# Optimization experiments

Measured on AMD Instinct MI355X. Metric: run time of the kernel, lower is better.

## Reference

```python
import jax, jax.numpy as jnp
import numpy as np

HID = 256  # LSTM hidden size hard-coded in the module


def _lstm_dir(x, wih, whh, b):
    # x: (N, T, I) -> (N, T, HID); PyTorch gate order i, f, g, o
    xw = jnp.einsum('nti,gi->ntg', x, wih) + b  # precompute input projection
    h0 = jnp.zeros((x.shape[0], whh.shape[1]), x.dtype)

    def step(carry, xt):
        h, c = carry
        g = xt + h @ whh.T
        i, f, gg, o = jnp.split(g, 4, axis=-1)
        c = jax.nn.sigmoid(f) * c + jax.nn.sigmoid(i) * jnp.tanh(gg)
        h = jax.nn.sigmoid(o) * jnp.tanh(c)
        return (h, c), h

    _, ys = jax.lax.scan(step, (h0, h0), jnp.swapaxes(xw, 0, 1))
    return jnp.swapaxes(ys, 0, 1)


def _bilstm(x, wf, uf, bf, wb, ub, bb):
    fwd = _lstm_dir(x, wf, uf, bf)
    bwd = _lstm_dir(x[:, ::-1], wb, ub, bb)[:, ::-1]
    return jnp.concatenate([fwd, bwd], axis=-1)  # (N, T, 2*HID)


def _renet2d(x, vp, hp, cw, cb):
    # Faithful to Renet2d.forward: vertical LSTM scans along W for each row of H,
    # horizontal LSTM scans along H for each column of W, then 1x1 conv.
    N, C, H, W = x.shape
    # original: transpose(1,3) then x[:,:,i,:] over H -> seq axis W, features C
    v_in = jnp.transpose(x, (0, 2, 3, 1)).reshape(N * H, W, C)
    v_out = _bilstm(v_in, *vp).reshape(N, H, W, 2 * HID)
    # torch.stack(temp, dim=2) -> (N, W, H, 512)
    s = jnp.transpose(v_out, (0, 2, 1, 3))
    h_in = s.reshape(N * W, H, 2 * HID)
    h_out = _bilstm(h_in, *hp).reshape(N, W, H, 2 * HID)
    # stack(dim=3) then transpose(1,2) -> (N, 512, H, W)
    y = jnp.transpose(h_out, (0, 3, 2, 1))
    return jnp.einsum('nchw,oc->nohw', y, cw) + cb[None, :, None, None]


def reference(x, v_wih_f, v_whh_f, v_b_f, v_wih_b, v_whh_b, v_b_b,
              h_wih_f, h_whh_f, h_b_f, h_wih_b, h_whh_b, h_b_b,
              c2_w, c2_b, c3_w, c3_b):
    vp = (v_wih_f, v_whh_f, v_b_f, v_wih_b, v_whh_b, v_b_b)
    hp = (h_wih_f, h_whh_f, h_b_f, h_wih_b, h_whh_b, h_b_b)
    B, C, D, H, W = x.shape
    r2d = lambda z: _renet2d(z, vp, hp, c2_w, c2_b)
    # NOTE: the source reuses Renet2d_D for all three stages (Renet2d_W/H are dead).
    # stage 1: python loop over D slicing dim 2 -> fold D into batch
    t = r2d(jnp.transpose(x, (0, 2, 1, 3, 4)).reshape(B * D, C, H, W)).reshape(B, D, C, H, W)
    x = jnp.transpose(t, (0, 2, 1, 3, 4))
    # stage 2: source loops range(w) but slices dim 3 (H); valid because H == W
    t = r2d(jnp.transpose(x, (0, 3, 1, 2, 4)).reshape(B * H, C, D, W)).reshape(B, H, C, D, W)
    x = jnp.transpose(t, (0, 2, 3, 1, 4))
    # stage 3: loops range(h) slicing dim 4 (W)
    t = r2d(jnp.transpose(x, (0, 4, 1, 2, 3)).reshape(B * W, C, D, H)).reshape(B, W, C, D, H)
    x = jnp.transpose(t, (0, 2, 3, 4, 1))
    # Conv3d 1x1x1
    return jnp.einsum('bcdhw,oc->bodhw', x, c3_w) + c3_b[None, :, None, None, None]


def setup_inputs() -> dict:
    key = jax.random.key(0)
    ks = jax.random.split(key, 17)
    B, C, S, O = 2, 64, 16, 64
    G = 4 * HID
    sc = 0.08

    def n(k, shape):
        return jax.random.normal(k, shape, jnp.float32) * sc

    return {
        'x': jax.random.normal(ks[0], (B, C, S, S, S), jnp.float32),
        # vertical LSTM (input C) fwd/bwd directions; b = b_ih + b_hh fused
        'v_wih_f': n(ks[1], (G, C)), 'v_whh_f': n(ks[2], (G, HID)), 'v_b_f': n(ks[3], (G,)),
        'v_wih_b': n(ks[4], (G, C)), 'v_whh_b': n(ks[5], (G, HID)), 'v_b_b': n(ks[6], (G,)),
        # horizontal LSTM (input 512)
        'h_wih_f': n(ks[7], (G, 2 * HID)), 'h_whh_f': n(ks[8], (G, HID)), 'h_b_f': n(ks[9], (G,)),
        'h_wih_b': n(ks[10], (G, 2 * HID)), 'h_whh_b': n(ks[11], (G, HID)), 'h_b_b': n(ks[12], (G,)),
        # Conv2d(512, in_channel, 1) inside Renet2d_D and Conv3d(in, out, 1)
        'c2_w': n(ks[13], (C, 2 * HID)), 'c2_b': n(ks[14], (C,)),
        'c3_w': n(ks[15], (O, C)), 'c3_b': n(ks[16], (O,)),
    }
```

## Files before the change

### kernel.cpp

```cpp
#include <hip/hip_runtime.h>
#include <hip/hip_bf16.h>
#include <hip/hip_fp16.h>


typedef __attribute__((ext_vector_type(8))) short bf16x8;
typedef __attribute__((ext_vector_type(4))) float f32x4;
typedef __attribute__((ext_vector_type(4))) unsigned int u32x4;
typedef __attribute__((ext_vector_type(2))) unsigned int u32x2;

#define AGENT __HIP_MEMORY_SCOPE_AGENT

__device__ __forceinline__ unsigned short f2bf(float f) {
    unsigned int u = __float_as_uint(f);
    u += 0x7fffu + ((u >> 16) & 1u);
    return (unsigned short)(u >> 16);
}

struct CastW { const float* src[9]; unsigned short* dst[9]; int n[9]; int L[9]; int perm[9]; };
__global__ void k_castw(CastW j) {
    const int a = blockIdx.y;
    const int i = blockIdx.x * 256 + threadIdx.x;
    if (i >= j.n[a]) return;
    const int L = j.L[a];
    const int r = i >> L, c = i & ((1 << L) - 1);
    const int dr = j.perm[a] ? ((r & 255) * 4 + (r >> 8)) : r;
    j.dst[a][(dr << L) | c] = f2bf(j.src[a][i]);
}
struct CastB { const float* src[4]; float* dst[4]; };
__global__ void k_castb(CastB j) {
    const int a = blockIdx.y;
    const int i = blockIdx.x * 256 + threadIdx.x;
    j.dst[a][(i & 255) * 4 + (i >> 8)] = j.src[a][i];
}

__global__ void k_gather(const float* __restrict__ X, unsigned short* __restrict__ vin,
                         int sm, int sa, int sb) {
    const int seq = blockIdx.x;
    const int n = seq >> 4, a = seq & 15;
    const size_t base = (size_t)(n >> 4) * 64 * 4096 + (size_t)sm * (n & 15) + (size_t)sa * a;
    for (int idx = threadIdx.x; idx < 1024; idx += 256) {
        const int c = idx & 63, b = idx >> 6;
        vin[((size_t)seq * 16 + b) * 64 + c] = f2bf(X[base + (size_t)c * 4096 + (size_t)sb * b]);
    }
}

__global__ __launch_bounds__(256) void k_gemm(const unsigned short* __restrict__ A, int K,
        const unsigned short* __restrict__ W0, const unsigned short* __restrict__ W1,
        const float* __restrict__ bias0, const float* __restrict__ bias1,
        __half* __restrict__ C, int ldc, int nvalid,
        int mode, float* __restrict__ out5d, int sm, int sa, int sb) {
    __shared__ unsigned short Alds[128 * 56];
    __shared__ unsigned short Blds[128 * 56];
    const unsigned short* W = blockIdx.z ? W1 : W0;
    const float* bias = blockIdx.z ? bias1 : bias0;
    C += (size_t)blockIdx.z * 8192 * ldc;
    const int m0 = blockIdx.x * 128, n0 = blockIdx.y * 128;
    const int tid = threadIdx.x;
    const int lane = tid & 63, wid = tid >> 6;
    const int wr = wid >> 1, wc = wid & 1;
    const int fl = lane & 15, kk = (lane >> 4) * 8;
    f32x4 acc[4][4];
    #pragma unroll
    for (int mi = 0; mi < 4; mi++)
        #pragma unroll
        for (int ni = 0; ni < 4; ni++) { f32x4 z = {0.f,0.f,0.f,0.f}; acc[mi][ni] = z; }

    for (int k0 = 0; k0 < K; k0 += 32) {
        __syncthreads();
        #pragma unroll
        for (int h = 0; h < 2; h++) {
            const int cid = tid + h * 256;
            const int row = cid >> 2, c4 = cid & 3;
            *(u32x4*)&Alds[row * 56 + c4 * 8] = *(const u32x4*)(A + (size_t)(m0 + row) * K + k0 + c4 * 8);
            *(u32x4*)&Blds[row * 56 + c4 * 8] = *(const u32x4*)(W + (size_t)(n0 + row) * K + k0 + c4 * 8);
        }
        __syncthreads();
        bf16x8 af[4], bfb[4];
        #pragma unroll
        for (int i = 0; i < 4; i++) {
            af[i]  = *(const bf16x8*)&Alds[(wr * 64 + i * 16 + fl) * 56 + kk];
            bfb[i] = *(const bf16x8*)&Blds[(wc * 64 + i * 16 + fl) * 56 + kk];
        }
        #pragma unroll
        for (int mi = 0; mi < 4; mi++)
            #pragma unroll
            for (int ni = 0; ni < 4; ni++)
                acc[mi][ni] = __builtin_amdgcn_mfma_f32_16x16x32_bf16(af[mi], bfb[ni], acc[mi][ni], 0, 0, 0);
    }
    const int rl = (lane >> 4) * 4;
    #pragma unroll
    for (int ni = 0; ni < 4; ni++) {
        const int col = n0 + wc * 64 + ni * 16 + fl;
        if (col < nvalid) {
            const float bs = bias[col];
            #pragma unroll
            for (int mi = 0; mi < 4; mi++) {
                const int row = m0 + wr * 64 + mi * 16 + rl;
                #pragma unroll
                for (int j = 0; j < 4; j++) {
                    const float v = acc[mi][ni][j] + bs;
                    if (mode) {
                        const int r = row + j;
                        const int n_ = r >> 8, b_ = (r >> 4) & 15, a_ = r & 15;
                        out5d[(size_t)(n_ >> 4) * 262144 + (size_t)sm * (n_ & 15) +
                              (size_t)sa * a_ + (size_t)sb * b_ + (size_t)col * 4096] = v;
                    } else {
                        C[(size_t)(row + j) * ldc + col] = __float2half(v);
                    }
                }
            }
        }
    }
}

__global__ __launch_bounds__(512, 2) void k_scan(const __half* __restrict__ xw,
        const unsigned short* __restrict__ whh_f, const unsigned short* __restrict__ whh_b,
        unsigned short* __restrict__ out, int out_mode,
        unsigned long long* __restrict__ HX, unsigned int* __restrict__ FLG, int phase) {
    __shared__ __align__(16) char gbuf[512 * 40];
    __shared__ __align__(16) char hbuf[16 * 512];
    const int tid = threadIdx.x;
    const int lane = tid & 63, w = tid >> 6;
    const int fl = lane & 15, fh = lane >> 4;
    const int st = blockIdx.x, dir = blockIdx.y, kh = blockIdx.z;
    const int seq0 = st * 16;
    const unsigned short* whh_k = (dir ? whh_b : whh_f) + (size_t)kh * 512 * 256;
    const __half* xwd = xw + (size_t)dir * (8192 * 1024);
    const int C0g = kh * 512 + w * 64;
    const int slot = ((dir * 32 + st) * 2 + kh);
    unsigned long long* hx_me = HX + (size_t)slot * 1024;
    const unsigned long long* hx_p = HX + (size_t)(slot ^ 1) * 1024;
    unsigned int* flg_me = FLG + slot * 64;
    unsigned int* flg_p  = FLG + (slot ^ 1) * 64;
    const unsigned int base = 16u * (unsigned int)phase;
    const int kOwnB = kh * 4;
    const int kParB = (1 - kh) * 4;

    #pragma unroll
    for (int i = 0; i < 4; i++) ((unsigned int*)hbuf)[tid + i * 512] = 0u;

    bf16x8 wown[4][4], wpar[4][4];
    #pragma unroll
    for (int nt = 0; nt < 4; nt++) {
        const unsigned short* rowp = whh_k + (size_t)(w * 64 + nt * 16 + fl) * 256 + fh * 8;
        #pragma unroll
        for (int i = 0; i < 4; i++) {
            wown[nt][i] = *(const bf16x8*)(rowp + (kOwnB + i) * 32);
            wpar[nt][i] = *(const bf16x8*)(rowp + (kParB + i) * 32);
        }
    }

    const int li = lane & 15, ls = lane >> 4;
    const int khalf = w * 16 + li;
    const int kglob = kh * 128 + khalf;
    float c_reg[4] = {0.f, 0.f, 0.f, 0.f};

    int tt = dir ? 15 : 0;
    const int tstep = dir ? -1 : 1;

    unsigned int xh[4][2], xhn[4][2];
    #pragma unroll
    for (int nt = 0; nt < 4; nt++)
        #pragma unroll
        for (int j2 = 0; j2 < 2; j2++) {
            const size_t b_ = ((size_t)(seq0 + fh * 4 + j2 * 2) * 16 + tt) * 1024 + C0g + nt * 16 + fl;
            const unsigned short h0 = __half_as_ushort(xwd[b_]);
            const unsigned short h1 = __half_as_ushort(xwd[b_ + 16 * 1024]);
            xh[nt][j2] = (unsigned int)h0 | ((unsigned int)h1 << 16);
        }

    __syncthreads();

    for (int t = 0; t < 16; t++) {
        if (t > 0) {
            const int ttp = tt - tstep;
            const int s = tid >> 5, q = tid & 31;
            const int ba = (s * 512 + (kh * 128 + q * 4) * 2) ^ ((s & 7) << 4);
            const u32x2 hv = *(const u32x2*)(hbuf + ba);
            const size_t row = out_mode ? ((size_t)(seq0 + s) * 16 + ttp)
                                        : ((size_t)st * 256 + (size_t)ttp * 16 + s);
            *(u32x2*)(out + row * 512 + dir * 256 + kh * 128 + q * 4) = hv;
        }
        bf16x8 afr[4];
        #pragma unroll
        for (int i = 0; i < 4; i++) {
            const int ba = (fl * 512 + (kOwnB + i) * 64 + fh * 16) ^ ((fl & 7) << 4);
            afr[i] = *(const bf16x8*)(hbuf + ba);
        }
        f32x4 acc[4];
        #pragma unroll
        for (int nt = 0; nt < 4; nt++) {
            acc[nt][0] = __half2float(__ushort_as_half((unsigned short)(xh[nt][0] & 0xffff)));
            acc[nt][1] = __half2float(__ushort_as_half((unsigned short)(xh[nt][0] >> 16)));
            acc[nt][2] = __half2float(__ushort_as_half((unsigned short)(xh[nt][1] & 0xffff)));
            acc[nt][3] = __half2float(__ushort_as_half((unsigned short)(xh[nt][1] >> 16)));
            #pragma unroll
            for (int i = 0; i < 4; i++)
                acc[nt] = __builtin_amdgcn_mfma_f32_16x16x32_bf16(afr[i], wown[nt][i], acc[nt], 0, 0, 0);
        }
        if (t > 0) {
            if (tid == 0) {
                const unsigned int want = base + (unsigned int)t;
                while (atomicAdd(flg_p, 0u) < want) __builtin_amdgcn_s_sleep(1);
            }
            asm volatile("s_barrier" ::: "memory");
            const unsigned long long pv =
                __hip_atomic_load(hx_p + (((t - 1) & 1) * 512 + tid), __ATOMIC_RELAXED, AGENT);
            const int kl = tid >> 2, sl0 = (tid & 3) * 4;
            const int kp = (1 - kh) * 128 + kl;
            #pragma unroll
            for (int e = 0; e < 4; e++) {
                const int s = sl0 + e;
                *(unsigned short*)(hbuf + ((s * 512 + kp * 2) ^ ((s & 7) << 4))) =
                    (unsigned short)(pv >> (16 * e));
            }
        }
        asm volatile("s_waitcnt lgkmcnt(0)\n\ts_barrier" ::: "memory");

        const int tn = (t < 15) ? tt + tstep : tt;
        #pragma unroll
        for (int nt = 0; nt < 4; nt++)
            #pragma unroll
            for (int j2 = 0; j2 < 2; j2++) {
                const size_t b_ = ((size_t)(seq0 + fh * 4 + j2 * 2) * 16 + tn) * 1024 + C0g + nt * 16 + fl;
                const unsigned short h0 = __half_as_ushort(xwd[b_]);
                const unsigned short h1 = __half_as_ushort(xwd[b_ + 16 * 1024]);
                xhn[nt][j2] = (unsigned int)h0 | ((unsigned int)h1 << 16);
            }

        #pragma unroll
        for (int i = 0; i < 4; i++) {
            const int ba = (fl * 512 + (kParB + i) * 64 + fh * 16) ^ ((fl & 7) << 4);
            afr[i] = *(const bf16x8*)(hbuf + ba);
        }
        #pragma unroll
        for (int nt = 0; nt < 4; nt++) {
            #pragma unroll
            for (int i = 0; i < 4; i++)
                acc[nt] = __builtin_amdgcn_mfma_f32_16x16x32_bf16(afr[i], wpar[nt][i], acc[nt], 0, 0, 0);
            const int coll = w * 64 + nt * 16 + fl;
            const unsigned int lo = (unsigned int)__half_as_ushort(__float2half(acc[nt][0])) |
                                    ((unsigned int)__half_as_ushort(__float2half(acc[nt][1])) << 16);
            const unsigned int hi = (unsigned int)__half_as_ushort(__float2half(acc[nt][2])) |
                                    ((unsigned int)__half_as_ushort(__float2half(acc[nt][3])) << 16);
            u32x2 pk = {lo, hi};
            *(u32x2*)(gbuf + coll * 40 + fh * 8) = pk;
        }

        float gv[4][4];
        const int colbase = w * 64 + 4 * li;
        #pragma unroll
        for (int g = 0; g < 4; g++) {
            const u32x2 a = *(const u32x2*)(gbuf + (colbase + g) * 40 + ls * 8);
            gv[g][0] = __half2float(__ushort_as_half((unsigned short)(a[0] & 0xffff)));
            gv[g][1] = __half2float(__ushort_as_half((unsigned short)(a[0] >> 16)));
            gv[g][2] = __half2float(__ushort_as_half((unsigned short)(a[1] & 0xffff)));
            gv[g][3] = __half2float(__ushort_as_half((unsigned short)(a[1] >> 16)));
        }
        unsigned long long hpack = 0ull;
        #pragma unroll
        for (int p2 = 0; p2 < 4; p2++) {
            const float ig = 1.f / (1.f + __expf(-gv[0][p2]));
            const float fg = 1.f / (1.f + __expf(-gv[1][p2]));
            const float e2 = __expf(2.f * gv[2][p2]);
            const float gg = 1.f - 2.f / (e2 + 1.f);
            const float og = 1.f / (1.f + __expf(-gv[3][p2]));
            const float c = fg * c_reg[p2] + ig * gg;
            c_reg[p2] = c;
            const float e2c = __expf(2.f * c);
            const float hv = og * (1.f - 2.f / (e2c + 1.f));
            const unsigned short hb = f2bf(hv);
            const int s = ls * 4 + p2;
            *(unsigned short*)(hbuf + ((s * 512 + kglob * 2) ^ ((s & 7) << 4))) = hb;
            hpack |= ((unsigned long long)hb) << (16 * p2);
        }

        if (t < 15)
            __hip_atomic_store(hx_me + ((t & 1) * 512 + khalf * 4 + ls), hpack, __ATOMIC_RELAXED, AGENT);
        #pragma unroll
        for (int nt = 0; nt < 4; nt++) { xh[nt][0] = xhn[nt][0]; xh[nt][1] = xhn[nt][1]; }
        tt = tn;
        __syncthreads();
        if (t < 15 && tid == 0)
            atomicExch(flg_me, base + (unsigned int)(t + 1));
    }
    {
        const int s = tid >> 5, q = tid & 31;
        const int ba = (s * 512 + (kh * 128 + q * 4) * 2) ^ ((s & 7) << 4);
        const u32x2 hv = *(const u32x2*)(hbuf + ba);
        const size_t row = out_mode ? ((size_t)(seq0 + s) * 16 + tt)
                                    : ((size_t)st * 256 + (size_t)tt * 16 + s);
        *(u32x2*)(out + row * 512 + dir * 256 + kh * 128 + q * 4) = hv;
    }
}

__global__ __launch_bounds__(256) void k_conv3f(const __half* __restrict__ CONV,
        const float* __restrict__ w, const float* __restrict__ bias, float* __restrict__ out) {
    __shared__ float xl[64 * 32];
    __shared__ float wl[64 * 64];
    const int bb = blockIdx.y;
    const int p0 = blockIdx.x * 32;
    const int tid = threadIdx.x;
    for (int i = tid; i < 64 * 32; i += 256) {
        const int c = i & 63, pp = i >> 6;
        const int p = p0 + pp;
        const int n_ = bb * 16 + (p & 15), b_ = (p >> 4) & 15, a_ = (p >> 8) & 15;
        const int r = (n_ * 16 + b_) * 16 + a_;
        xl[c * 32 + pp] = __half2float(CONV[(size_t)r * 64 + c]);
    }
    for (int i = tid; i < 64 * 64; i += 256) wl[i] = w[i];
    __syncthreads();
    const int pp = tid & 31, og = tid >> 5;
    #pragma unroll
    for (int oj = 0; oj < 8; oj++) {
        const int o = og * 8 + oj;
        float acc = bias[o];
        #pragma unroll 16
        for (int c = 0; c < 64; c++) acc += xl[c * 32 + pp] * wl[o * 64 + c];
        out[((size_t)bb * 64 + o) * 4096 + p0 + pp] = acc;
    }
}

extern "C" void kernel_launch(void* const* d_in, const int* in_sizes, int n_in,
                              void* d_out, int out_size, void* d_ws, size_t ws_size,
                              hipStream_t stream) {
    (void)in_sizes; (void)n_in; (void)out_size; (void)ws_size;
    const float* x     = (const float*)d_in[0];
    const float* vwihf = (const float*)d_in[1];
    const float* vwhhf = (const float*)d_in[2];
    const float* vbf   = (const float*)d_in[3];
    const float* vwihb = (const float*)d_in[4];
    const float* vwhhb = (const float*)d_in[5];
    const float* vbb   = (const float*)d_in[6];
    const float* hwihf = (const float*)d_in[7];
    const float* hwhhf = (const float*)d_in[8];
    const float* hbf   = (const float*)d_in[9];
    const float* hwihb = (const float*)d_in[10];
    const float* hwhhb = (const float*)d_in[11];
    const float* hbb   = (const float*)d_in[12];
    const float* c2w   = (const float*)d_in[13];
    const float* c2b   = (const float*)d_in[14];
    const float* c3w   = (const float*)d_in[15];
    const float* c3b   = (const float*)d_in[16];

    char* p = (char*)d_ws;
    auto alloc = [&](size_t bytes) { char* r = p; p += (bytes + 255) & ~((size_t)255); return r; };
    unsigned short* bVWIHf = (unsigned short*)alloc((size_t)1024 * 64 * 2);
    unsigned short* bVWIHb = (unsigned short*)alloc((size_t)1024 * 64 * 2);
    unsigned short* bVWHHf = (unsigned short*)alloc((size_t)1024 * 256 * 2);
    unsigned short* bVWHHb = (unsigned short*)alloc((size_t)1024 * 256 * 2);
    unsigned short* bHWIHf = (unsigned short*)alloc((size_t)1024 * 512 * 2);
    unsigned short* bHWIHb = (unsigned short*)alloc((size_t)1024 * 512 * 2);
    unsigned short* bHWHHf = (unsigned short*)alloc((size_t)1024 * 256 * 2);
    unsigned short* bHWHHb = (unsigned short*)alloc((size_t)1024 * 256 * 2);
    unsigned short* bC2W   = (unsigned short*)alloc((size_t)128 * 512 * 2);
    float* pVBf = (float*)alloc(1024 * 4);
    float* pVBb = (float*)alloc(1024 * 4);
    float* pHBf = (float*)alloc(1024 * 4);
    float* pHBb = (float*)alloc(1024 * 4);
    unsigned long long* HX = (unsigned long long*)alloc((size_t)128 * 8192);
    unsigned int* FLG = (unsigned int*)alloc((size_t)128 * 256);
    float* XA = (float*)alloc((size_t)524288 * 4);
    float* XB = (float*)alloc((size_t)524288 * 4);
    unsigned short* VIN = (unsigned short*)alloc((size_t)8192 * 64 * 2);
    __half* XW = (__half*)alloc((size_t)2 * 8192 * 1024 * 2);
    unsigned short* S_   = (unsigned short*)alloc((size_t)8192 * 512 * 2);
    unsigned short* HOUT = (unsigned short*)alloc((size_t)8192 * 512 * 2);
    __half* CONV = (__half*)VIN;

    hipMemsetAsync(bC2W, 0, (size_t)128 * 512 * 2, stream);
    hipMemsetAsync(FLG, 0, (size_t)128 * 256, stream);
    CastW cw;
    const float* srcs[9] = {vwihf, vwihb, vwhhf, vwhhb, hwihf, hwihb, hwhhf, hwhhb, c2w};
    unsigned short* dsts[9] = {bVWIHf, bVWIHb, bVWHHf, bVWHHb, bHWIHf, bHWIHb, bHWHHf, bHWHHb, bC2W};
    const int ns[9] = {65536, 65536, 262144, 262144, 524288, 524288, 262144, 262144, 32768};
    const int Ls[9] = {6, 6, 8, 8, 9, 9, 8, 8, 9};
    const int pm[9] = {1, 1, 1, 1, 1, 1, 1, 1, 0};
    for (int i = 0; i < 9; i++) { cw.src[i] = srcs[i]; cw.dst[i] = dsts[i]; cw.n[i] = ns[i]; cw.L[i] = Ls[i]; cw.perm[i] = pm[i]; }
    k_castw<<<dim3(2048, 9), 256, 0, stream>>>(cw);
    CastB cb;
    cb.src[0] = vbf; cb.dst[0] = pVBf;
    cb.src[1] = vbb; cb.dst[1] = pVBb;
    cb.src[2] = hbf; cb.dst[2] = pHBf;
    cb.src[3] = hbb; cb.dst[3] = pHBb;
    k_castb<<<dim3(4, 4), 256, 0, stream>>>(cb);

    const int SMs[3] = {256, 16, 1}, SAs[3] = {16, 256, 256}, SBs[3] = {1, 1, 16};
    for (int s = 0; s < 3; s++) {
        const float* Xin = (s == 0) ? x : ((s == 1) ? XA : XB);
        float* Xout = (s == 0) ? XA : XB;
        k_gather<<<512, 256, 0, stream>>>(Xin, VIN, SMs[s], SAs[s], SBs[s]);
        k_gemm<<<dim3(64, 8, 2), 256, 0, stream>>>(VIN, 64, bVWIHf, bVWIHb, pVBf, pVBb,
                                                   XW, 1024, 1024, 0, nullptr, 0, 0, 0);
        k_scan<<<dim3(32, 2, 2), 512, 0, stream>>>(XW, bVWHHf, bVWHHb, S_, 0, HX, FLG, s * 2 + 0);
        k_gemm<<<dim3(64, 8, 2), 256, 0, stream>>>(S_, 512, bHWIHf, bHWIHb, pHBf, pHBb,
                                                   XW, 1024, 1024, 0, nullptr, 0, 0, 0);
        k_scan<<<dim3(32, 2, 2), 512, 0, stream>>>(XW, bHWHHf, bHWHHb, HOUT, 1, HX, FLG, s * 2 + 1);
        if (s < 2)
            k_gemm<<<dim3(64, 1, 1), 256, 0, stream>>>(HOUT, 512, bC2W, bC2W, c2b, c2b,
                                                       CONV, 64, 64, 1, Xout, SMs[s], SAs[s], SBs[s]);
        else
            k_gemm<<<dim3(64, 1, 1), 256, 0, stream>>>(HOUT, 512, bC2W, bC2W, c2b, c2b,
                                                       CONV, 64, 64, 0, nullptr, 0, 0, 0);
    }
    k_conv3f<<<dim3(128, 2), 256, 0, stream>>>(CONV, c3w, c3b, (float*)d_out);
}
```

Before: 591.0 us.

## Add producer warp for cross-block h exchange in LSTM scan; async LDS loads in GEMM

The scan kernel gains a ninth wavefront that waits on the partner block's flag, reads its half of the hidden state and writes it into a double-buffered LDS h buffer, signalling compute waves through a per-step shared flag instead of a block-wide barrier. The intent is to overlap the inter-block handoff latency with the own-half MFMA work and the input prefetch. Separately, the GEMM tile loads switch to global_load_lds with an XOR swizzle instead of padded register-staged copies. Risks include the spin-wait on LDS flags, the barrier count matching between producer and compute waves, and occupancy dropping to one 576-thread block per CU.

```diff
diff --git a/kernel.cpp b/kernel.cpp
--- a/kernel.cpp
+++ b/kernel.cpp
@@ -14,6 +14,10 @@
     unsigned int u = __float_as_uint(f);
     u += 0x7fffu + ((u >> 16) & 1u);
     return (unsigned short)(u >> 16);
+}
+__device__ __forceinline__ void gload16(const void* g, void* l) {
+    __builtin_amdgcn_global_load_lds((const __attribute__((address_space(1))) unsigned int*)g,
+                                     (__attribute__((address_space(3))) unsigned int*)l, 16, 0, 0);
 }
 
 struct CastW { const float* src[9]; unsigned short* dst[9]; int n[9]; int L[9]; int perm[9]; };
@@ -49,8 +53,8 @@
         const float* __restrict__ bias0, const float* __restrict__ bias1,
         __half* __restrict__ C, int ldc, int nvalid,
         int mode, float* __restrict__ out5d, int sm, int sa, int sb) {
-    __shared__ unsigned short Alds[128 * 56];
-    __shared__ unsigned short Blds[128 * 56];
+    __shared__ unsigned short Alds[128 * 32];
+    __shared__ unsigned short Blds[128 * 32];
     const unsigned short* W = blockIdx.z ? W1 : W0;
     const float* bias = blockIdx.z ? bias1 : bias0;
     C += (size_t)blockIdx.z * 8192 * ldc;
@@ -58,28 +62,29 @@
     const int tid = threadIdx.x;
     const int lane = tid & 63, wid = tid >> 6;
     const int wr = wid >> 1, wc = wid & 1;
-    const int fl = lane & 15, kk = (lane >> 4) * 8;
+    const int fl = lane & 15, fh = lane >> 4;
     f32x4 acc[4][4];
     #pragma unroll
     for (int mi = 0; mi < 4; mi++)
         #pragma unroll
         for (int ni = 0; ni < 4; ni++) { f32x4 z = {0.f,0.f,0.f,0.f}; acc[mi][ni] = z; }
 
+    const int srow = wid * 32 + (lane >> 2);
+    const int swz = ((lane & 3) ^ ((lane >> 2) & 3)) * 8;
+
     for (int k0 = 0; k0 < K; k0 += 32) {
         __syncthreads();
-        #pragma unroll
-        for (int h = 0; h < 2; h++) {
-            const int cid = tid + h * 256;
-            const int row = cid >> 2, c4 = cid & 3;
-            *(u32x4*)&Alds[row * 56 + c4 * 8] = *(const u32x4*)(A + (size_t)(m0 + row) * K + k0 + c4 * 8);
-            *(u32x4*)&Blds[row * 56 + c4 * 8] = *(const u32x4*)(W + (size_t)(n0 + row) * K + k0 + c4 * 8);
-        }
+        gload16(A + (size_t)(m0 + srow) * K + k0 + swz,      &Alds[(wid * 32) * 32]);
+        gload16(A + (size_t)(m0 + srow + 16) * K + k0 + swz, &Alds[(wid * 32 + 16) * 32]);
+        gload16(W + (size_t)(n0 + srow) * K + k0 + swz,      &Blds[(wid * 32) * 32]);
+        gload16(W + (size_t)(n0 + srow + 16) * K + k0 + swz, &Blds[(wid * 32 + 16) * 32]);
         __syncthreads();
         bf16x8 af[4], bfb[4];
+        const int rc = (fh ^ (fl & 3)) * 8;
         #pragma unroll
         for (int i = 0; i < 4; i++) {
-            af[i]  = *(const bf16x8*)&Alds[(wr * 64 + i * 16 + fl) * 56 + kk];
-            bfb[i] = *(const bf16x8*)&Blds[(wc * 64 + i * 16 + fl) * 56 + kk];
+            af[i]  = *(const bf16x8*)&Alds[(wr * 64 + i * 16 + fl) * 32 + rc];
+            bfb[i] = *(const bf16x8*)&Blds[(wc * 64 + i * 16 + fl) * 32 + rc];
         }
         #pragma unroll
         for (int mi = 0; mi < 4; mi++)
@@ -87,7 +92,7 @@
             for (int ni = 0; ni < 4; ni++)
                 acc[mi][ni] = __builtin_amdgcn_mfma_f32_16x16x32_bf16(af[mi], bfb[ni], acc[mi][ni], 0, 0, 0);
     }
-    const int rl = (lane >> 4) * 4;
+    const int rl = fh * 4;
     #pragma unroll
     for (int ni = 0; ni < 4; ni++) {
         const int col = n0 + wc * 64 + ni * 16 + fl;
@@ -113,12 +118,13 @@
     }
 }
 
-__global__ __launch_bounds__(512, 2) void k_scan(const __half* __restrict__ xw,
+__global__ __launch_bounds__(576, 1) void k_scan(const __half* __restrict__ xw,
         const unsigned short* __restrict__ whh_f, const unsigned short* __restrict__ whh_b,
         unsigned short* __restrict__ out, int out_mode,
         unsigned long long* __restrict__ HX, unsigned int* __restrict__ FLG, int phase) {
     __shared__ __align__(16) char gbuf[512 * 40];
-    __shared__ __align__(16) char hbuf[16 * 512];
+    __shared__ __align__(16) char hbuf[2 * 8192];
+    __shared__ int sflag[16];
     const int tid = threadIdx.x;
     const int lane = tid & 63, w = tid >> 6;
     const int fl = lane & 15, fh = lane >> 4;
@@ -126,7 +132,6 @@
     const int seq0 = st * 16;
     const unsigned short* whh_k = (dir ? whh_b : whh_f) + (size_t)kh * 512 * 256;
     const __half* xwd = xw + (size_t)dir * (8192 * 1024);
-    const int C0g = kh * 512 + w * 64;
     const int slot = ((dir * 32 + st) * 2 + kh);
     unsigned long long* hx_me = HX + (size_t)slot * 1024;
     const unsigned long long* hx_p = HX + (size_t)(slot ^ 1) * 1024;
@@ -136,18 +141,67 @@
     const int kOwnB = kh * 4;
     const int kParB = (1 - kh) * 4;
 
-    #pragma unroll
-    for (int i = 0; i < 4; i++) ((unsigned int*)hbuf)[tid + i * 512] = 0u;
+    if (tid < 16) sflag[tid] = 0;
+    for (int i = tid; i < 2048; i += 576) ((unsigned int*)(hbuf + 8192))[i] = 0u;
 
     bf16x8 wown[4][4], wpar[4][4];
-    #pragma unroll
-    for (int nt = 0; nt < 4; nt++) {
-        const unsigned short* rowp = whh_k + (size_t)(w * 64 + nt * 16 + fl) * 256 + fh * 8;
-        #pragma unroll
-        for (int i = 0; i < 4; i++) {
-            wown[nt][i] = *(const bf16x8*)(rowp + (kOwnB + i) * 32);
-            wpar[nt][i] = *(const bf16x8*)(rowp + (kParB + i) * 32);
-        }
+    unsigned int xh[4][2], xhn[4][2];
+    const int C0g = kh * 512 + w * 64;
+    int tt = dir ? 15 : 0;
+    const int tstep = dir ? -1 : 1;
+    if (w < 8) {
+        #pragma unroll
+        for (int nt = 0; nt < 4; nt++) {
+            const unsigned short* rowp = whh_k + (size_t)(w * 64 + nt * 16 + fl) * 256 + fh * 8;
+            #pragma unroll
+            for (int i = 0; i < 4; i++) {
+                wown[nt][i] = *(const bf16x8*)(rowp + (kOwnB + i) * 32);
+                wpar[nt][i] = *(const bf16x8*)(rowp + (kParB + i) * 32);
+            }
+        }
+        #pragma unroll
+        for (int nt = 0; nt < 4; nt++)
+            #pragma unroll
+            for (int j2 = 0; j2 < 2; j2++) {
+                const size_t b_ = ((size_t)(seq0 + fh * 4 + j2 * 2) * 16 + tt) * 1024 + C0g + nt * 16 + fl;
+                const unsigned short h0 = __half_as_ushort(xwd[b_]);
+                const unsigned short h1 = __half_as_ushort(xwd[b_ + 16 * 1024]);
+                xh[nt][j2] = (unsigned int)h0 | ((unsigned int)h1 << 16);
+            }
+    }
+    __syncthreads();
+
+    if (w == 8) {
+        for (int t = 0; t < 16; t++) {
+            if (t > 0) {
+                if (lane == 0) {
+                    const unsigned int want = base + (unsigned int)t;
+                    while (atomicAdd(flg_p, 0u) < want) __builtin_amdgcn_s_sleep(1);
+                }
+                const unsigned long long* src = hx_p + ((t - 1) & 1) * 512;
+                unsigned long long pv[8];
+                #pragma unroll
+                for (int e = 0; e < 8; e++)
+                    pv[e] = __hip_atomic_load(src + lane + e * 64, __ATOMIC_RELAXED, AGENT);
+                char* hwbuf = hbuf + ((t - 1) & 1) * 8192;
+                #pragma unroll
+                for (int e = 0; e < 8; e++) {
+                    const int idx = lane + e * 64;
+                    const int kl = idx >> 2, sl0 = (idx & 3) * 4;
+                    const int kp = (1 - kh) * 128 + kl;
+                    #pragma unroll
+                    for (int e2 = 0; e2 < 4; e2++) {
+                        const int s = sl0 + e2;
+                        *(unsigned short*)(hwbuf + ((s * 512 + kp * 2) ^ ((s & 7) << 4))) =
+                            (unsigned short)(pv[e] >> (16 * e2));
+                    }
+                }
+                asm volatile("s_waitcnt lgkmcnt(0)" ::: "memory");
+                if (lane == 0) *(volatile int*)&sflag[t] = 1;
+            }
+            __syncthreads();
+        }
+        return;
     }
 
     const int li = lane & 15, ls = lane >> 4;
@@ -155,28 +209,14 @@
     const int kglob = kh * 128 + khalf;
     float c_reg[4] = {0.f, 0.f, 0.f, 0.f};
 
-    int tt = dir ? 15 : 0;
-    const int tstep = dir ? -1 : 1;
-
-    unsigned int xh[4][2], xhn[4][2];
-    #pragma unroll
-    for (int nt = 0; nt < 4; nt++)
-        #pragma unroll
-        for (int j2 = 0; j2 < 2; j2++) {
-            const size_t b_ = ((size_t)(seq0 + fh * 4 + j2 * 2) * 16 + tt) * 1024 + C0g + nt * 16 + fl;
-            const unsigned short h0 = __half_as_ushort(xwd[b_]);
-            const unsigned short h1 = __half_as_ushort(xwd[b_ + 16 * 1024]);
-            xh[nt][j2] = (unsigned int)h0 | ((unsigned int)h1 << 16);
-        }
-
-    __syncthreads();
-
     for (int t = 0; t < 16; t++) {
+        const char* hread = hbuf + ((t - 1) & 1) * 8192;
+        char* hwr = hbuf + (t & 1) * 8192;
         if (t > 0) {
             const int ttp = tt - tstep;
             const int s = tid >> 5, q = tid & 31;
             const int ba = (s * 512 + (kh * 128 + q * 4) * 2) ^ ((s & 7) << 4);
-            const u32x2 hv = *(const u32x2*)(hbuf + ba);
+            const u32x2 hv = *(const u32x2*)(hread + ba);
             const size_t row = out_mode ? ((size_t)(seq0 + s) * 16 + ttp)
                                         : ((size_t)st * 256 + (size_t)ttp * 16 + s);
             *(u32x2*)(out + row * 512 + dir * 256 + kh * 128 + q * 4) = hv;
@@ -185,7 +225,7 @@
         #pragma unroll
         for (int i = 0; i < 4; i++) {
             const int ba = (fl * 512 + (kOwnB + i) * 64 + fh * 16) ^ ((fl & 7) << 4);
-            afr[i] = *(const bf16x8*)(hbuf + ba);
+            afr[i] = *(const bf16x8*)(hread + ba);
         }
         f32x4 acc[4];
         #pragma unroll
@@ -198,25 +238,6 @@
             for (int i = 0; i < 4; i++)
                 acc[nt] = __builtin_amdgcn_mfma_f32_16x16x32_bf16(afr[i], wown[nt][i], acc[nt], 0, 0, 0);
         }
-        if (t > 0) {
-            if (tid == 0) {
-                const unsigned int want = base + (unsigned int)t;
-                while (atomicAdd(flg_p, 0u) < want) __builtin_amdgcn_s_sleep(1);
-            }
-            asm volatile("s_barrier" ::: "memory");
-            const unsigned long long pv =
-                __hip_atomic_load(hx_p + (((t - 1) & 1) * 512 + tid), __ATOMIC_RELAXED, AGENT);
-            const int kl = tid >> 2, sl0 = (tid & 3) * 4;
-            const int kp = (1 - kh) * 128 + kl;
-            #pragma unroll
-            for (int e = 0; e < 4; e++) {
-                const int s = sl0 + e;
-                *(unsigned short*)(hbuf + ((s * 512 + kp * 2) ^ ((s & 7) << 4))) =
-                    (unsigned short)(pv >> (16 * e));
-            }
-        }
-        asm volatile("s_waitcnt lgkmcnt(0)\n\ts_barrier" ::: "memory");
-
         const int tn = (t < 15) ? tt + tstep : tt;
         #pragma unroll
         for (int nt = 0; nt < 4; nt++)
@@ -227,11 +248,15 @@
                 const unsigned short h1 = __half_as_ushort(xwd[b_ + 16 * 1024]);
                 xhn[nt][j2] = (unsigned int)h0 | ((unsigned int)h1 << 16);
             }
-
+        if (t > 0) {
+            volatile int* sf = (volatile int*)&sflag[t];
+            while (*sf == 0) { }
+            asm volatile("" ::: "memory");
+        }
         #pragma unroll
         for (int i = 0; i < 4; i++) {
             const int ba = (fl * 512 + (kParB + i) * 64 + fh * 16) ^ ((fl & 7) << 4);
-            afr[i] = *(const bf16x8*)(hbuf + ba);
+            afr[i] = *(const bf16x8*)(hread + ba);
         }
         #pragma unroll
         for (int nt = 0; nt < 4; nt++) {
@@ -246,7 +271,6 @@
             u32x2 pk = {lo, hi};
             *(u32x2*)(gbuf + coll * 40 + fh * 8) = pk;
         }
-
         float gv[4][4];
         const int colbase = w * 64 + 4 * li;
         #pragma unroll
@@ -271,10 +295,9 @@
             const float hv = og * (1.f - 2.f / (e2c + 1.f));
             const unsigned short hb = f2bf(hv);
             const int s = ls * 4 + p2;
-            *(unsigned short*)(hbuf + ((s * 512 + kglob * 2) ^ ((s & 7) << 4))) = hb;
+            *(unsigned short*)(hwr + ((s * 512 + kglob * 2) ^ ((s & 7) << 4))) = hb;
             hpack |= ((unsigned long long)hb) << (16 * p2);
         }
-
         if (t < 15)
             __hip_atomic_store(hx_me + ((t & 1) * 512 + khalf * 4 + ls), hpack, __ATOMIC_RELAXED, AGENT);
         #pragma unroll
@@ -287,7 +310,7 @@
     {
         const int s = tid >> 5, q = tid & 31;
         const int ba = (s * 512 + (kh * 128 + q * 4) * 2) ^ ((s & 7) << 4);
-        const u32x2 hv = *(const u32x2*)(hbuf + ba);
+        const u32x2 hv = *(const u32x2*)(hbuf + 8192 + ba);
         const size_t row = out_mode ? ((size_t)(seq0 + s) * 16 + tt)
                                     : ((size_t)st * 256 + (size_t)tt * 16 + s);
         *(u32x2*)(out + row * 512 + dir * 256 + kh * 128 + q * 4) = hv;
@@ -392,10 +415,10 @@
         k_gather<<<512, 256, 0, stream>>>(Xin, VIN, SMs[s], SAs[s], SBs[s]);
         k_gemm<<<dim3(64, 8, 2), 256, 0, stream>>>(VIN, 64, bVWIHf, bVWIHb, pVBf, pVBb,
                                                    XW, 1024, 1024, 0, nullptr, 0, 0, 0);
-        k_scan<<<dim3(32, 2, 2), 512, 0, stream>>>(XW, bVWHHf, bVWHHb, S_, 0, HX, FLG, s * 2 + 0);
+        k_scan<<<dim3(32, 2, 2), 576, 0, stream>>>(XW, bVWHHf, bVWHHb, S_, 0, HX, FLG, s * 2 + 0);
         k_gemm<<<dim3(64, 8, 2), 256, 0, stream>>>(S_, 512, bHWIHf, bHWIHb, pHBf, pHBb,
                                                    XW, 1024, 1024, 0, nullptr, 0, 0, 0);
-        k_scan<<<dim3(32, 2, 2), 512, 0, stream>>>(XW, bHWHHf, bHWHHb, HOUT, 1, HX, FLG, s * 2 + 1);
+        k_scan<<<dim3(32, 2, 2), 576, 0, stream>>>(XW, bHWHHf, bHWHHb, HOUT, 1, HX, FLG, s * 2 + 1);
         if (s < 2)
             k_gemm<<<dim3(64, 1, 1), 256, 0, stream>>>(HOUT, 512, bC2W, bC2W, c2b, c2b,
                                                        CONV, 64, 64, 1, Xout, SMs[s], SAs[s], SBs[s]);
```

After: 799.1 us. 1.35x slower.

## Use direct global-to-LDS loads with XOR swizzle in GEMM; tile gather via LDS

Applied to the files above, without the earlier changes.

The GEMM tile loads now use global_load_lds (16-byte direct-to-LDS) into an unpadded LDS layout. An XOR swizzle is applied on both the load and the fragment read to avoid bank conflicts, which removes the register round-trip and shrinks the LDS footprint. The gather kernel now stages the transposed bf16 data through shared memory so that global writes are coalesced 8-byte stores instead of scattered 2-byte stores. The direct-load path depends on per-wave contiguous LDS placement matching the swizzle, so any indexing mistake would silently corrupt results.

```diff
diff --git a/kernel.cpp b/kernel.cpp
--- a/kernel.cpp
+++ b/kernel.cpp
@@ -14,6 +14,10 @@
     unsigned int u = __float_as_uint(f);
     u += 0x7fffu + ((u >> 16) & 1u);
     return (unsigned short)(u >> 16);
+}
+__device__ __forceinline__ void gload16(const void* g, void* l) {
+    __builtin_amdgcn_global_load_lds((const __attribute__((address_space(1))) unsigned int*)g,
+                                     (__attribute__((address_space(3))) unsigned int*)l, 16, 0, 0);
 }
 
 struct CastW { const float* src[9]; unsigned short* dst[9]; int n[9]; int L[9]; int perm[9]; };
@@ -35,13 +39,24 @@
 
 __global__ void k_gather(const float* __restrict__ X, unsigned short* __restrict__ vin,
                          int sm, int sa, int sb) {
+    __shared__ unsigned short sd[16 * 68];
     const int seq = blockIdx.x;
     const int n = seq >> 4, a = seq & 15;
     const size_t base = (size_t)(n >> 4) * 64 * 4096 + (size_t)sm * (n & 15) + (size_t)sa * a;
-    for (int idx = threadIdx.x; idx < 1024; idx += 256) {
-        const int c = idx & 63, b = idx >> 6;
-        vin[((size_t)seq * 16 + b) * 64 + c] = f2bf(X[base + (size_t)c * 4096 + (size_t)sb * b]);
-    }
+    const int t = threadIdx.x;
+    #pragma unroll
+    for (int j = 0; j < 4; j++) {
+        const int i = t + j * 256;
+        const int c = i >> 4, b = i & 15;
+        sd[b * 68 + c] = f2bf(X[base + (size_t)c * 4096 + (size_t)sb * b]);
+    }
+    __syncthreads();
+    const int r = t >> 4, c0 = (t & 15) * 4;
+    unsigned long long v;
+    unsigned short* sp = &sd[r * 68 + c0];
+    v = (unsigned long long)sp[0] | ((unsigned long long)sp[1] << 16) |
+        ((unsigned long long)sp[2] << 32) | ((unsigned long long)sp[3] << 48);
+    *(unsigned long long*)(vin + (size_t)seq * 1024 + r * 64 + c0) = v;
 }
 
 __global__ __launch_bounds__(256) void k_gemm(const unsigned short* __restrict__ A, int K,
@@ -49,8 +64,8 @@
         const float* __restrict__ bias0, const float* __restrict__ bias1,
         __half* __restrict__ C, int ldc, int nvalid,
         int mode, float* __restrict__ out5d, int sm, int sa, int sb) {
-    __shared__ unsigned short Alds[128 * 56];
-    __shared__ unsigned short Blds[128 * 56];
+    __shared__ unsigned short Alds[128 * 32];
+    __shared__ unsigned short Blds[128 * 32];
     const unsigned short* W = blockIdx.z ? W1 : W0;
     const float* bias = blockIdx.z ? bias1 : bias0;
     C += (size_t)blockIdx.z * 8192 * ldc;
@@ -58,28 +73,29 @@
     const int tid = threadIdx.x;
     const int lane = tid & 63, wid = tid >> 6;
     const int wr = wid >> 1, wc = wid & 1;
-    const int fl = lane & 15, kk = (lane >> 4) * 8;
+    const int fl = lane & 15, fh = lane >> 4;
     f32x4 acc[4][4];
     #pragma unroll
     for (int mi = 0; mi < 4; mi++)
         #pragma unroll
         for (int ni = 0; ni < 4; ni++) { f32x4 z = {0.f,0.f,0.f,0.f}; acc[mi][ni] = z; }
+
+    const int srow = wid * 32 + (lane >> 2);
+    const int swz = ((lane & 3) ^ ((lane >> 2) & 3)) * 8;
 
     for (int k0 = 0; k0 < K; k0 += 32) {
         __syncthreads();
-        #pragma unroll
-        for (int h = 0; h < 2; h++) {
-            const int cid = tid + h * 256;
-            const int row = cid >> 2, c4 = cid & 3;
-            *(u32x4*)&Alds[row * 56 + c4 * 8] = *(const u32x4*)(A + (size_t)(m0 + row) * K + k0 + c4 * 8);
-            *(u32x4*)&Blds[row * 56 + c4 * 8] = *(const u32x4*)(W + (size_t)(n0 + row) * K + k0 + c4 * 8);
-        }
+        gload16(A + (size_t)(m0 + srow) * K + k0 + swz,      &Alds[(wid * 32) * 32]);
+        gload16(A + (size_t)(m0 + srow + 16) * K + k0 + swz, &Alds[(wid * 32 + 16) * 32]);
+        gload16(W + (size_t)(n0 + srow) * K + k0 + swz,      &Blds[(wid * 32) * 32]);
+        gload16(W + (size_t)(n0 + srow + 16) * K + k0 + swz, &Blds[(wid * 32 + 16) * 32]);
         __syncthreads();
         bf16x8 af[4], bfb[4];
+        const int rc = (fh ^ (fl & 3)) * 8;
         #pragma unroll
         for (int i = 0; i < 4; i++) {
-            af[i]  = *(const bf16x8*)&Alds[(wr * 64 + i * 16 + fl) * 56 + kk];
-            bfb[i] = *(const bf16x8*)&Blds[(wc * 64 + i * 16 + fl) * 56 + kk];
+            af[i]  = *(const bf16x8*)&Alds[(wr * 64 + i * 16 + fl) * 32 + rc];
+            bfb[i] = *(const bf16x8*)&Blds[(wc * 64 + i * 16 + fl) * 32 + rc];
         }
         #pragma unroll
         for (int mi = 0; mi < 4; mi++)
@@ -87,7 +103,7 @@
             for (int ni = 0; ni < 4; ni++)
                 acc[mi][ni] = __builtin_amdgcn_mfma_f32_16x16x32_bf16(af[mi], bfb[ni], acc[mi][ni], 0, 0, 0);
     }
-    const int rl = (lane >> 4) * 4;
+    const int rl = fh * 4;
     #pragma unroll
     for (int ni = 0; ni < 4; ni++) {
         const int col = n0 + wc * 64 + ni * 16 + fl;
```

New measurement: 585.6 us. No clear change (-0.9%).
